# Kernel tuning notes

Hardware: AMD Instinct MI355X
Metric: run time of the kernel (lower is better)

Reference implementation:

```python
import jax, jax.numpy as jnp
import numpy as np

DIM = 2048
NUM_HEADS = 16
HEAD_DIM = 128


def setup_inputs() -> dict:
    key = jax.random.key(0)
    ks = jax.random.split(key, 9)
    B, S = 2, 2048
    s = lambda fan_in: 1.0 / np.sqrt(fan_in)
    return {
        "x": jax.random.normal(ks[0], (B, S, DIM), dtype=jnp.float32),
        "Wq": jax.random.uniform(ks[1], (DIM, NUM_HEADS * HEAD_DIM), jnp.float32, -s(DIM), s(DIM)),
        "bq": jax.random.uniform(ks[2], (NUM_HEADS * HEAD_DIM,), jnp.float32, -s(DIM), s(DIM)),
        "Wk": jax.random.uniform(ks[3], (DIM, HEAD_DIM), jnp.float32, -s(DIM), s(DIM)),
        "bk": jax.random.uniform(ks[4], (HEAD_DIM,), jnp.float32, -s(DIM), s(DIM)),
        "Wv": jax.random.uniform(ks[5], (DIM, HEAD_DIM), jnp.float32, -s(DIM), s(DIM)),
        "bv": jax.random.uniform(ks[6], (HEAD_DIM,), jnp.float32, -s(DIM), s(DIM)),
        "Wo": jax.random.uniform(ks[7], (NUM_HEADS * HEAD_DIM, DIM), jnp.float32, -s(NUM_HEADS * HEAD_DIM), s(NUM_HEADS * HEAD_DIM)),
        "bo": jax.random.uniform(ks[8], (DIM,), jnp.float32, -s(NUM_HEADS * HEAD_DIM), s(NUM_HEADS * HEAD_DIM)),
    }


def reference(x, Wq, bq, Wk, bk, Wv, bv, Wo, bo):
    B, S, _ = x.shape
    H, D = NUM_HEADS, HEAD_DIM
    q = (x @ Wq + bq).reshape(B, S, H, D)          # bnhd
    k = x @ Wk + bk                                 # bmd (single shared KV head)
    v = x @ Wv + bv                                 # bmd
    scale = 1.0 / np.sqrt(D).astype(np.float32)
    scores = jnp.einsum('bnhd,bmd->bnhm', q, k) * scale  # [B,S,H,S]
    attn = jax.nn.softmax(scores, axis=-1)
    out = jnp.einsum('bnhm,bmd->bnhd', attn, v)
    out = out.reshape(B, S, H * D)
    return out @ Wo + bo
```

## Files before the change

### kernel.cpp

```cpp
#include <hip/hip_runtime.h>
#include <cstdint>


#define SEQ 2048
#define NQKV 2304
#define MTOT 4096

typedef __attribute__((ext_vector_type(8))) short bf16x8;
typedef __attribute__((ext_vector_type(4))) float f32x4;
typedef __attribute__((ext_vector_type(16))) float f32x16;

__device__ __forceinline__ unsigned short cvt_bf16(float f) {
  union { float f; unsigned int u; } v; v.f = f;
  unsigned int r = v.u + 0x7FFFu + ((v.u >> 16) & 1u);
  return (unsigned short)(r >> 16);
}

__device__ __forceinline__ unsigned cvt_pk_bf16(float lo, float hi_) {
  unsigned r;
  asm("v_cvt_pk_bf16_f32 %0, %1, %2" : "=v"(r) : "v"(lo), "v"(hi_));
  return r;
}

__device__ __forceinline__ void plane_swap(unsigned &a, unsigned &b) {
  asm volatile("v_permlane32_swap_b32 %0, %1" : "+v"(a), "+v"(b));
}

__device__ __forceinline__ float exp2_(float x) {
#if __has_builtin(__builtin_amdgcn_exp2f)
  return __builtin_amdgcn_exp2f(x);
#else
  return exp2f(x);
#endif
}

typedef const __attribute__((address_space(1))) void gvoid;
typedef __attribute__((address_space(3))) void lvoid;
__device__ __forceinline__ void gload16(const void* g, void* l) {
  __builtin_amdgcn_global_load_lds((gvoid*)g, (lvoid*)l, 16, 0, 0);
}


__global__ __launch_bounds__(256) void cast_x_kernel(const float* __restrict__ x,
                                                     unsigned short* __restrict__ o) {
  long long i = ((long long)blockIdx.x * 256 + threadIdx.x) * 8;
  float4 a = *(const float4*)(x + i);
  float4 b = *(const float4*)(x + i + 4);
  union { bf16x8 v; unsigned short u[8]; } r;
  r.u[0] = cvt_bf16(a.x); r.u[1] = cvt_bf16(a.y); r.u[2] = cvt_bf16(a.z); r.u[3] = cvt_bf16(a.w);
  r.u[4] = cvt_bf16(b.x); r.u[5] = cvt_bf16(b.y); r.u[6] = cvt_bf16(b.z); r.u[7] = cvt_bf16(b.w);
  *(bf16x8*)(o + i) = r.v;
}

__global__ __launch_bounds__(256) void transpose_cast(
    const float* __restrict__ s0, const float* __restrict__ s1, const float* __restrict__ s2,
    int n1, int n2, int st0, int st1, int st2,
    unsigned short* __restrict__ dst, int K) {
  __shared__ float t[32][33];
  int n0 = blockIdx.x * 32, k0 = blockIdx.y * 32;
  const float* src; int off, stride;
  if (n0 < n1)      { src = s0; off = 0;  stride = st0; }
  else if (n0 < n2) { src = s1; off = n1; stride = st1; }
  else              { src = s2; off = n2; stride = st2; }
  int tx = threadIdx.x & 31, ty = threadIdx.x >> 5;
  #pragma unroll
  for (int r = 0; r < 4; r++)
    t[ty + r * 8][tx] = src[(size_t)(k0 + ty + r * 8) * stride + (n0 - off) + tx];
  __syncthreads();
  #pragma unroll
  for (int r = 0; r < 4; r++)
    dst[(size_t)(n0 + ty + r * 8) * K + k0 + tx] = cvt_bf16(t[tx][ty + r * 8]);
}

__global__ __launch_bounds__(256) void concat_bias(const float* __restrict__ bq,
    const float* __restrict__ bk, const float* __restrict__ bv, float* __restrict__ b1) {
  int i = blockIdx.x * 256 + threadIdx.x;
  if (i < NQKV) b1[i] = (i < 2048) ? bq[i] : (i < 2176 ? bk[i - 2048] : bv[i - 2176]);
}

__global__ __launch_bounds__(256) void kfrag_prep(const unsigned short* __restrict__ qkv,
                                                  unsigned short* __restrict__ kfrag) {
  int gid = blockIdx.x * 4 + (threadIdx.x >> 6);
  int l = threadIdx.x & 63;
  int b = gid >> 9, rem = gid & 511;
  int jt = rem >> 3, kt = rem & 7;
  const unsigned short* src = qkv + (size_t)(b * 2048 + jt * 32 + (l & 31)) * NQKV
                              + 2048 + kt * 16 + (l >> 5) * 8;
  *(bf16x8*)(kfrag + (size_t)gid * 512 + l * 8) = *(const bf16x8*)src;
}

__global__ __launch_bounds__(256) void vfrag_prep(const unsigned short* __restrict__ qkv,
                                                  unsigned short* __restrict__ vfrag) {
  int gid = blockIdx.x * 4 + (threadIdx.x >> 6);
  int l = threadIdx.x & 63;
  int b = gid >> 9, rem = gid & 511;
  int jt = rem >> 3, s = (rem >> 2) & 1, d0 = rem & 3;
  union { bf16x8 v; unsigned short u[8]; } o;
  #pragma unroll
  for (int e = 0; e < 8; e++)
    o.u[e] = qkv[(size_t)(b * 2048 + jt * 32 + s * 16 + (l >> 5) * 8 + e) * NQKV
                 + 2176 + d0 * 32 + (l & 31)];
  *(bf16x8*)(vfrag + (size_t)gid * 512 + l * 8) = o.v;
}

template <int BF16_OUT>
__global__ __launch_bounds__(256) void gemm_bt(const unsigned short* __restrict__ A,
    const unsigned short* __restrict__ BT, const float* __restrict__ bias,
    void* __restrict__ Cout, int N) {
  __shared__ unsigned short As[128 * 32];
  __shared__ unsigned short Bs[128 * 32];
  const int tid = threadIdx.x;
  const int l = tid & 63, w = tid >> 6;
  const int l15 = l & 15, g = l >> 4;
  const int wr = w >> 1, wc = w & 1;
  const int brow = blockIdx.x * 128, bcol = blockIdx.y * 128;
  const int K = 2048;
  const unsigned short* ga = A + (size_t)(brow + w * 32 + (l >> 2)) * K + (l & 3) * 8;
  const unsigned short* gb = BT + (size_t)(bcol + w * 32 + (l >> 2)) * K + (l & 3) * 8;
  unsigned short* lA = &As[w * 1024];
  unsigned short* lB = &Bs[w * 1024];
  f32x4 acc[4][4];
  const f32x4 z = {0.f, 0.f, 0.f, 0.f};
  #pragma unroll
  for (int i = 0; i < 4; i++)
    #pragma unroll
    for (int j = 0; j < 4; j++) acc[i][j] = z;

  for (int kt = 0; kt < K; kt += 32) {
    gload16(ga + kt, lA);
    gload16(ga + kt + 16 * K, lA + 512);
    gload16(gb + kt, lB);
    gload16(gb + kt + 16 * K, lB + 512);
    __syncthreads();
    bf16x8 af[4], bfr[4];
    #pragma unroll
    for (int mi = 0; mi < 4; mi++)
      af[mi] = *(const bf16x8*)&As[(wr * 64 + mi * 16 + l15) * 32 + g * 8];
    #pragma unroll
    for (int ni = 0; ni < 4; ni++)
      bfr[ni] = *(const bf16x8*)&Bs[(wc * 64 + ni * 16 + l15) * 32 + g * 8];
    __syncthreads();
    #pragma unroll
    for (int mi = 0; mi < 4; mi++)
      #pragma unroll
      for (int ni = 0; ni < 4; ni++)
        acc[mi][ni] = __builtin_amdgcn_mfma_f32_16x16x32_bf16(af[mi], bfr[ni], acc[mi][ni], 0, 0, 0);
  }
  float* Cf = (float*)Cout;
  unsigned short* Cb = (unsigned short*)Cout;
  #pragma unroll
  for (int ni = 0; ni < 4; ni++) {
    int col = bcol + wc * 64 + ni * 16 + l15;
    float bv = bias[col];
    #pragma unroll
    for (int mi = 0; mi < 4; mi++) {
      int row = brow + wr * 64 + mi * 16 + g * 4;
      #pragma unroll
      for (int r = 0; r < 4; r++) {
        float v = acc[mi][ni][r] + bv;
        if (BF16_OUT) Cb[(size_t)(row + r) * N + col] = cvt_bf16(v);
        else          Cf[(size_t)(row + r) * N + col] = v;
      }
    }
  }
}

__global__ __launch_bounds__(64, 1) void attn_kernel(
    const unsigned short* __restrict__ qkv, const unsigned short* __restrict__ kfrag,
    const unsigned short* __restrict__ vfrag, unsigned short* __restrict__ aout) {
  const int l = threadIdx.x, l31 = l & 31, hi = l >> 5;
  const int bid = blockIdx.x;
  const int qt = bid & 31, h = (bid >> 5) & 15, b = bid >> 9;
  const float C2 = 0.12752299126446508f;

  bf16x8 qf[2][8];
  #pragma unroll
  for (int q2 = 0; q2 < 2; q2++) {
    const unsigned short* qp =
        qkv + (size_t)(b * 2048 + qt * 64 + q2 * 32 + l31) * NQKV + h * 128 + hi * 8;
    #pragma unroll
    for (int kt = 0; kt < 8; kt++) qf[q2][kt] = *(const bf16x8*)(qp + kt * 16);
  }
  const unsigned short* kp = kfrag + (size_t)b * 262144 + l * 8;
  const unsigned short* vp = vfrag + (size_t)b * 262144 + l * 8;

  f32x16 acc[2][4];
  #pragma unroll
  for (int q2 = 0; q2 < 2; q2++)
    #pragma unroll
    for (int d0 = 0; d0 < 4; d0++)
      #pragma unroll
      for (int r = 0; r < 16; r++) acc[q2][d0][r] = 0.f;
  float mrun[2] = {-3.0e38f, -3.0e38f}, lsum[2] = {0.f, 0.f};

  bf16x8 ka[8], kb2[8], vr[8];
  #pragma unroll
  for (int u = 0; u < 8; u++) ka[u] = *(const bf16x8*)(kp + u * 512);

#define SOFT_PV(STV, Q2, jtv)                                                   \
  do {                                                                          \
    float vmax = -3.0e38f;                                                      \
    _Pragma("unroll")                                                           \
    for (int r = 0; r < 16; r++) vmax = fmaxf(vmax, STV[r]);                    \
    vmax = fmaxf(vmax, __shfl_xor(vmax, 32));                                   \
    if ((jtv) == 0) {                                                           \
      mrun[Q2] = vmax;                                                          \
    } else if (!__all((vmax - mrun[Q2]) * C2 <= 8.0f)) {                        \
      float mn_ = fmaxf(mrun[Q2], vmax);                                        \
      float al_ = exp2_((mrun[Q2] - mn_) * C2);                                 \
      mrun[Q2] = mn_; lsum[Q2] *= al_;                                          \
      _Pragma("unroll")                                                         \
      for (int r = 0; r < 16; r++) {                                            \
        float av_ = __shfl(al_, (r & 3) + 8 * (r >> 2) + 4 * hi);               \
        _Pragma("unroll")                                                       \
        for (int d0 = 0; d0 < 4; d0++) acc[Q2][d0][r] *= av_;                   \
      }                                                                         \
    }                                                                           \
    const float mc_ = mrun[Q2] * C2;                                            \
    float rs_ = 0.f;                                                            \
    _Pragma("unroll")                                                           \
    for (int r = 0; r < 16; r++) { STV[r] = exp2_(STV[r] * C2 - mc_); rs_ += STV[r]; } \
    rs_ += __shfl_xor(rs_, 32);                                                 \
    lsum[Q2] += rs_;                                                            \
    _Pragma("unroll")                                                           \
    for (int s = 0; s < 2; s++) {                                               \
      unsigned a0_ = cvt_pk_bf16(STV[s * 8 + 0], STV[s * 8 + 1]);               \
      unsigned b0_ = cvt_pk_bf16(STV[s * 8 + 4], STV[s * 8 + 5]);               \
      plane_swap(a0_, b0_);                                                     \
      unsigned a1_ = cvt_pk_bf16(STV[s * 8 + 2], STV[s * 8 + 3]);               \
      unsigned b1_ = cvt_pk_bf16(STV[s * 8 + 6], STV[s * 8 + 7]);               \
      plane_swap(a1_, b1_);                                                     \
      union { bf16x8 v; unsigned u[4]; } pa_;                                   \
      pa_.u[0] = a0_; pa_.u[1] = a1_; pa_.u[2] = b0_; pa_.u[3] = b1_;           \
      _Pragma("unroll")                                                         \
      for (int d0 = 0; d0 < 4; d0++)                                            \
        acc[Q2][d0] = __builtin_amdgcn_mfma_f32_32x32x16_bf16(pa_.v, vr[s * 4 + d0], acc[Q2][d0], 0, 0, 0); \
    }                                                                           \
  } while (0)

#define ATTN_TILE(KC, KN, jtv)                                                  \
  do {                                                                          \
    const int jn_ = ((jtv) < 63) ? (jtv) + 1 : 63;                              \
    _Pragma("unroll")                                                           \
    for (int u = 0; u < 8; u++)                                                 \
      vr[u] = *(const bf16x8*)(vp + (size_t)(jtv) * 4096 + u * 512);            \
    _Pragma("unroll")                                                           \
    for (int u = 0; u < 8; u++)                                                 \
      KN[u] = *(const bf16x8*)(kp + (size_t)jn_ * 4096 + u * 512);              \
    f32x16 se0, so0, se1, so1;                                                  \
    _Pragma("unroll")                                                           \
    for (int r = 0; r < 16; r++) { se0[r] = 0.f; so0[r] = 0.f; se1[r] = 0.f; so1[r] = 0.f; } \
    _Pragma("unroll")                                                           \
    for (int kt = 0; kt < 4; kt++) {                                            \
      se0 = __builtin_amdgcn_mfma_f32_32x32x16_bf16(KC[2 * kt], qf[0][2 * kt], se0, 0, 0, 0); \
      so0 = __builtin_amdgcn_mfma_f32_32x32x16_bf16(KC[2 * kt + 1], qf[0][2 * kt + 1], so0, 0, 0, 0); \
      se1 = __builtin_amdgcn_mfma_f32_32x32x16_bf16(KC[2 * kt], qf[1][2 * kt], se1, 0, 0, 0); \
      so1 = __builtin_amdgcn_mfma_f32_32x32x16_bf16(KC[2 * kt + 1], qf[1][2 * kt + 1], so1, 0, 0, 0); \
    }                                                                           \
    float stv0[16], stv1[16];                                                   \
    _Pragma("unroll")                                                           \
    for (int r = 0; r < 16; r++) { stv0[r] = se0[r] + so0[r]; stv1[r] = se1[r] + so1[r]; } \
    SOFT_PV(stv0, 0, jtv);                                                      \
    SOFT_PV(stv1, 1, jtv);                                                      \
  } while (0)

  for (int jt2 = 0; jt2 < 32; jt2++) {
    ATTN_TILE(ka, kb2, 2 * jt2);
    ATTN_TILE(kb2, ka, 2 * jt2 + 1);
  }
#undef ATTN_TILE
#undef SOFT_PV

  #pragma unroll
  for (int q2 = 0; q2 < 2; q2++) {
    float linv = 1.0f / lsum[q2];
    const int qrow0 = b * 2048 + qt * 64 + q2 * 32;
    #pragma unroll
    for (int r = 0; r < 16; r++) {
      const int crow = (r & 3) + 8 * (r >> 2) + 4 * hi;
      float li = __shfl(linv, crow);
      size_t rbase = (size_t)(qrow0 + crow) * 2048 + h * 128 + l31;
      #pragma unroll
      for (int d0 = 0; d0 < 4; d0++)
        aout[rbase + d0 * 32] = cvt_bf16(acc[q2][d0][r] * li);
    }
  }
}


extern "C" void kernel_launch(void* const* d_in, const int* in_sizes, int n_in,
                              void* d_out, int out_size, void* d_ws, size_t ws_size,
                              hipStream_t stream) {
  const float* x  = (const float*)d_in[0];
  const float* Wq = (const float*)d_in[1];
  const float* bq = (const float*)d_in[2];
  const float* Wk = (const float*)d_in[3];
  const float* bk = (const float*)d_in[4];
  const float* Wv = (const float*)d_in[5];
  const float* bv = (const float*)d_in[6];
  const float* Wo = (const float*)d_in[7];
  const float* bo = (const float*)d_in[8];
  float* out = (float*)d_out;

  char* ws = (char*)d_ws;
  size_t off = 0;
  auto alloc = [&](size_t bytes) -> void* {
    void* p = ws + off;
    off += (bytes + 255) & ~(size_t)255;
    return p;
  };
  unsigned short* xb     = (unsigned short*)alloc((size_t)MTOT * 2048 * 2);
  unsigned short* W1T    = (unsigned short*)alloc((size_t)NQKV * 2048 * 2);
  unsigned short* WoT    = (unsigned short*)alloc((size_t)2048 * 2048 * 2);
  float*          bias1  = (float*)alloc((size_t)NQKV * 4);
  unsigned short* qkv    = (unsigned short*)alloc((size_t)MTOT * NQKV * 2);
  unsigned short* kfragb = (unsigned short*)alloc((size_t)2 * 262144 * 2);
  unsigned short* vfragb = (unsigned short*)alloc((size_t)2 * 262144 * 2);
  unsigned short* aoutb  = (unsigned short*)alloc((size_t)MTOT * 2048 * 2);
  if (off > ws_size) return;

  cast_x_kernel<<<4096, 256, 0, stream>>>(x, xb);
  transpose_cast<<<dim3(72, 64), 256, 0, stream>>>(Wq, Wk, Wv, 2048, 2176,
                                                   2048, 128, 128, W1T, 2048);
  transpose_cast<<<dim3(64, 64), 256, 0, stream>>>(Wo, Wo, Wo, 2048, 2048,
                                                   2048, 2048, 2048, WoT, 2048);
  concat_bias<<<9, 256, 0, stream>>>(bq, bk, bv, bias1);

  gemm_bt<1><<<dim3(32, 18), 256, 0, stream>>>(xb, W1T, bias1, qkv, NQKV);
  kfrag_prep<<<256, 256, 0, stream>>>(qkv, kfragb);
  vfrag_prep<<<256, 256, 0, stream>>>(qkv, vfragb);
  attn_kernel<<<1024, 64, 0, stream>>>(qkv, kfragb, vfragb, aoutb);
  gemm_bt<0><<<dim3(32, 16), 256, 0, stream>>>(aoutb, WoT, bo, out, 2048);
}
```

Before: 206.8 us.

## Software-pipeline attention loop: overlap next QK^T MFMAs with current softmax/PV

Restructures the flash-attention inner loop so the QK^T MFMAs for tile j+1 are issued before the PV MFMAs for tile j, with softmax of tile j+1 following. K and V are double-buffered and prefetched two tiles ahead. The aim is to hide the softmax VALU/exp latency and global-load latency behind matrix-core work. It costs extra registers for the second V buffer, the stored P fragments and live score accumulators, which may increase spilling or lower occupancy.

```diff
diff --git a/kernel.cpp b/kernel.cpp
--- a/kernel.cpp
+++ b/kernel.cpp
@@ -193,83 +193,89 @@
       for (int r = 0; r < 16; r++) acc[q2][d0][r] = 0.f;
   float mrun[2] = {-3.0e38f, -3.0e38f}, lsum[2] = {0.f, 0.f};
 
-  bf16x8 ka[8], kb2[8], vr[8];
-  #pragma unroll
-  for (int u = 0; u < 8; u++) ka[u] = *(const bf16x8*)(kp + u * 512);
-
-#define SOFT_PV(STV, Q2, jtv)                                                   \
-  do {                                                                          \
-    float vmax = -3.0e38f;                                                      \
-    _Pragma("unroll")                                                           \
-    for (int r = 0; r < 16; r++) vmax = fmaxf(vmax, STV[r]);                    \
-    vmax = fmaxf(vmax, __shfl_xor(vmax, 32));                                   \
-    if ((jtv) == 0) {                                                           \
-      mrun[Q2] = vmax;                                                          \
-    } else if (!__all((vmax - mrun[Q2]) * C2 <= 8.0f)) {                        \
-      float mn_ = fmaxf(mrun[Q2], vmax);                                        \
-      float al_ = exp2_((mrun[Q2] - mn_) * C2);                                 \
-      mrun[Q2] = mn_; lsum[Q2] *= al_;                                          \
-      _Pragma("unroll")                                                         \
-      for (int r = 0; r < 16; r++) {                                            \
-        float av_ = __shfl(al_, (r & 3) + 8 * (r >> 2) + 4 * hi);               \
-        _Pragma("unroll")                                                       \
-        for (int d0 = 0; d0 < 4; d0++) acc[Q2][d0][r] *= av_;                   \
-      }                                                                         \
-    }                                                                           \
-    const float mc_ = mrun[Q2] * C2;                                            \
-    float rs_ = 0.f;                                                            \
-    _Pragma("unroll")                                                           \
-    for (int r = 0; r < 16; r++) { STV[r] = exp2_(STV[r] * C2 - mc_); rs_ += STV[r]; } \
-    rs_ += __shfl_xor(rs_, 32);                                                 \
-    lsum[Q2] += rs_;                                                            \
-    _Pragma("unroll")                                                           \
-    for (int s = 0; s < 2; s++) {                                               \
-      unsigned a0_ = cvt_pk_bf16(STV[s * 8 + 0], STV[s * 8 + 1]);               \
-      unsigned b0_ = cvt_pk_bf16(STV[s * 8 + 4], STV[s * 8 + 5]);               \
-      plane_swap(a0_, b0_);                                                     \
-      unsigned a1_ = cvt_pk_bf16(STV[s * 8 + 2], STV[s * 8 + 3]);               \
-      unsigned b1_ = cvt_pk_bf16(STV[s * 8 + 6], STV[s * 8 + 7]);               \
-      plane_swap(a1_, b1_);                                                     \
-      union { bf16x8 v; unsigned u[4]; } pa_;                                   \
-      pa_.u[0] = a0_; pa_.u[1] = a1_; pa_.u[2] = b0_; pa_.u[3] = b1_;           \
-      _Pragma("unroll")                                                         \
-      for (int d0 = 0; d0 < 4; d0++)                                            \
-        acc[Q2][d0] = __builtin_amdgcn_mfma_f32_32x32x16_bf16(pa_.v, vr[s * 4 + d0], acc[Q2][d0], 0, 0, 0); \
-    }                                                                           \
-  } while (0)
-
-#define ATTN_TILE(KC, KN, jtv)                                                  \
-  do {                                                                          \
-    const int jn_ = ((jtv) < 63) ? (jtv) + 1 : 63;                              \
-    _Pragma("unroll")                                                           \
-    for (int u = 0; u < 8; u++)                                                 \
-      vr[u] = *(const bf16x8*)(vp + (size_t)(jtv) * 4096 + u * 512);            \
-    _Pragma("unroll")                                                           \
-    for (int u = 0; u < 8; u++)                                                 \
-      KN[u] = *(const bf16x8*)(kp + (size_t)jn_ * 4096 + u * 512);              \
-    f32x16 se0, so0, se1, so1;                                                  \
-    _Pragma("unroll")                                                           \
+  bf16x8 ka[8], kb2[8], va8[8], vb8[8];
+  bf16x8 pa_v[2][2];
+  f32x16 se0, so0, se1, so1;
+
+#define LOADK(DST, T_) { _Pragma("unroll")                                     \
+    for (int u = 0; u < 8; u++)                                                \
+      DST[u] = *(const bf16x8*)(kp + (size_t)(T_) * 4096 + u * 512); }
+#define LOADV(DST, T_) { _Pragma("unroll")                                     \
+    for (int u = 0; u < 8; u++)                                                \
+      DST[u] = *(const bf16x8*)(vp + (size_t)(T_) * 4096 + u * 512); }
+
+#define QK2(KC) {                                                              \
+    _Pragma("unroll")                                                          \
     for (int r = 0; r < 16; r++) { se0[r] = 0.f; so0[r] = 0.f; se1[r] = 0.f; so1[r] = 0.f; } \
-    _Pragma("unroll")                                                           \
-    for (int kt = 0; kt < 4; kt++) {                                            \
+    _Pragma("unroll")                                                          \
+    for (int kt = 0; kt < 4; kt++) {                                           \
       se0 = __builtin_amdgcn_mfma_f32_32x32x16_bf16(KC[2 * kt], qf[0][2 * kt], se0, 0, 0, 0); \
       so0 = __builtin_amdgcn_mfma_f32_32x32x16_bf16(KC[2 * kt + 1], qf[0][2 * kt + 1], so0, 0, 0, 0); \
       se1 = __builtin_amdgcn_mfma_f32_32x32x16_bf16(KC[2 * kt], qf[1][2 * kt], se1, 0, 0, 0); \
       so1 = __builtin_amdgcn_mfma_f32_32x32x16_bf16(KC[2 * kt + 1], qf[1][2 * kt + 1], so1, 0, 0, 0); \
-    }                                                                           \
-    float stv0[16], stv1[16];                                                   \
-    _Pragma("unroll")                                                           \
-    for (int r = 0; r < 16; r++) { stv0[r] = se0[r] + so0[r]; stv1[r] = se1[r] + so1[r]; } \
-    SOFT_PV(stv0, 0, jtv);                                                      \
-    SOFT_PV(stv1, 1, jtv);                                                      \
-  } while (0)
-
-  for (int jt2 = 0; jt2 < 32; jt2++) {
-    ATTN_TILE(ka, kb2, 2 * jt2);
-    ATTN_TILE(kb2, ka, 2 * jt2 + 1);
-  }
-#undef ATTN_TILE
-#undef SOFT_PV
+    } }
+
+#define PV2(VB) { _Pragma("unroll")                                            \
+    for (int s = 0; s < 2; s++) {                                              \
+      _Pragma("unroll")                                                        \
+      for (int d0 = 0; d0 < 4; d0++) {                                         \
+        acc[0][d0] = __builtin_amdgcn_mfma_f32_32x32x16_bf16(pa_v[0][s], VB[s * 4 + d0], acc[0][d0], 0, 0, 0); \
+        acc[1][d0] = __builtin_amdgcn_mfma_f32_32x32x16_bf16(pa_v[1][s], VB[s * 4 + d0], acc[1][d0], 0, 0, 0); \
+      } } }
+
+#define SM1(SE, SO, Q2, FIRST) {                                               \
+    float stv[16]; float vmax = -3.0e38f;                                      \
+    _Pragma("unroll")                                                          \
+    for (int r = 0; r < 16; r++) { stv[r] = SE[r] + SO[r]; vmax = fmaxf(vmax, stv[r]); } \
+    vmax = fmaxf(vmax, __shfl_xor(vmax, 32));                                  \
+    if (FIRST) { mrun[Q2] = vmax; }                                            \
+    else if (!__all((vmax - mrun[Q2]) * C2 <= 8.0f)) {                         \
+      float mn_ = fmaxf(mrun[Q2], vmax);                                       \
+      float al_ = exp2_((mrun[Q2] - mn_) * C2);                                \
+      mrun[Q2] = mn_; lsum[Q2] *= al_;                                         \
+      _Pragma("unroll")                                                        \
+      for (int r = 0; r < 16; r++) {                                           \
+        float av_ = __shfl(al_, (r & 3) + 8 * (r >> 2) + 4 * hi);              \
+        _Pragma("unroll")                                                      \
+        for (int d0 = 0; d0 < 4; d0++) acc[Q2][d0][r] *= av_;                  \
+      } }                                                                      \
+    const float mc_ = mrun[Q2] * C2;                                           \
+    float rs_ = 0.f;                                                           \
+    _Pragma("unroll")                                                          \
+    for (int r = 0; r < 16; r++) { stv[r] = exp2_(stv[r] * C2 - mc_); rs_ += stv[r]; } \
+    rs_ += __shfl_xor(rs_, 32);                                                \
+    lsum[Q2] += rs_;                                                           \
+    _Pragma("unroll")                                                          \
+    for (int s = 0; s < 2; s++) {                                              \
+      unsigned a0_ = cvt_pk_bf16(stv[s * 8 + 0], stv[s * 8 + 1]);              \
+      unsigned b0_ = cvt_pk_bf16(stv[s * 8 + 4], stv[s * 8 + 5]);              \
+      plane_swap(a0_, b0_);                                                    \
+      unsigned a1_ = cvt_pk_bf16(stv[s * 8 + 2], stv[s * 8 + 3]);              \
+      unsigned b1_ = cvt_pk_bf16(stv[s * 8 + 6], stv[s * 8 + 7]);              \
+      plane_swap(a1_, b1_);                                                    \
+      union { bf16x8 v; unsigned u[4]; } pa_;                                  \
+      pa_.u[0] = a0_; pa_.u[1] = a1_; pa_.u[2] = b0_; pa_.u[3] = b1_;          \
+      pa_v[Q2][s] = pa_.v;                                                     \
+    } }
+#define SM2(FIRST) { SM1(se0, so0, 0, FIRST); SM1(se1, so1, 1, FIRST); }
+
+  LOADK(ka, 0); LOADK(kb2, 1); LOADV(va8, 0); LOADV(vb8, 1);
+  QK2(ka); SM2(true);
+
+  for (int jt2 = 0; jt2 < 31; jt2++) {
+    const int t0 = 2 * jt2;
+    QK2(kb2); PV2(va8); LOADK(ka, t0 + 2); LOADV(va8, t0 + 2); SM2(false);
+    QK2(ka); PV2(vb8); LOADK(kb2, t0 + 3); LOADV(vb8, t0 + 3); SM2(false);
+  }
+  QK2(kb2); PV2(va8); SM2(false);
+  PV2(vb8);
+
+#undef LOADK
+#undef LOADV
+#undef QK2
+#undef PV2
+#undef SM1
+#undef SM2
 
   #pragma unroll
   for (int q2 = 0; q2 < 2; q2++) {
```

Result: no change. 206.3 us (-0.3%).
